# Performance work log

Measured on AMD Instinct MI355X. Metric: run time of the kernel, lower is better.

## Reference

```python
import jax, jax.numpy as jnp
import numpy as np

B, H, S, W, F = 16, 4, 8, 256, 16


def setup_inputs() -> dict:
    key = jax.random.key(0)
    kx, kk = jax.random.split(key)
    x = jax.random.normal(kx, (B, S, W, F), dtype=jnp.float32)
    kernel = jax.random.normal(kk, (H, S, S, W), dtype=jnp.float32)
    return {"x": x, "kernel": kernel}


def reference(x, kernel):
    # kernel: [H, S, S, W]; x: [B, S, W, F]
    Hh, Ss, _, Ww = kernel.shape
    r = jnp.arange(Ww)
    # stacked[h,x,y,j,i] = roll(kernel, shifts=j+1)[i] = kernel[(i-(j+1)) % W]
    idx = (r[None, :] - (r[:, None] + 1)) % Ww          # [W(row=j), W(col=i)]
    stacked = kernel[..., idx]                            # [H,S,S,W,W]
    # torch.tril over last two dims: keep col i <= row j
    tri = (r[None, :] <= r[:, None])                      # [W,W]
    stacked = jnp.where(tri, stacked, jnp.zeros((), dtype=stacked.dtype))
    # masked triangular time-mix contraction
    out = jnp.einsum('hxyji,bxif->bhxyjf', stacked, x)    # [B,H,S,S,W,F]
    base = jnp.arange(1, Ww + 1, dtype=out.dtype).reshape(1, 1, 1, 1, Ww, 1)
    out = out / base
    # transform_x: on diagonal series (x==y) roll time dim by 1, zero first step
    diag_mod = jnp.roll(out, 1, axis=4)
    not_first = (r != 0).reshape(1, 1, 1, 1, Ww, 1)
    diag_mod = diag_mod * not_first.astype(out.dtype)
    eye = jnp.eye(Ss, dtype=bool).reshape(1, 1, Ss, Ss, 1, 1)
    return jnp.where(eye, diag_mod, out)
```

## Files before the change

kernel.cpp:

```cpp
#include <hip/hip_runtime.h>
#include <hip/hip_bf16.h>

typedef short short8 __attribute__((ext_vector_type(8)));
typedef float f32x4 __attribute__((ext_vector_type(4)));

union FragAB { unsigned long long l[2]; int i[4]; short8 v; };

__global__ __launch_bounds__(256, 2)
void k_fused(const float* __restrict__ x,
             const float* __restrict__ kern,
             float* __restrict__ out)
{
    __shared__ __align__(16) ushort Xts[128 * 264];
    __shared__ __align__(8)  ushort wforL[2][4][336];

    const int blk = blockIdx.x;
    const int id = blk & 255;
    const int c  = id & 15;
    const int nt = (id >> 4) & 1;
    const int sx = id >> 5;
    const int mt = blk >> 8;

    const int t = threadIdx.x;

    #pragma unroll
    for (int e2 = 0; e2 < 2; ++e2) {
        const int hy = c * 2 + e2;
        const int h = hy >> 3, sy = hy & 7;
        const float* krow = kern + ((h * 8 + sx) * 8 + sy) * 256;
        #pragma unroll
        for (int s = 0; s < 4; ++s) {
            #pragma unroll
            for (int pass = 0; pass < 2; ++pass) {
                int q = t + pass * 256;
                if (q < 336) {
                    int src = q - s;
                    float v = (src >= 0 && src < 256) ? krow[src] : 0.0f;
                    __hip_bfloat16 hv = __float2bfloat16(v);
                    wforL[e2][s][q] = reinterpret_cast<ushort&>(hv);
                }
            }
        }
    }

    {
        const float4* xbase = reinterpret_cast<const float4*>(x);
        const int b0 = nt * 8;
        #pragma unroll
        for (int it = 0; it < 16; ++it) {
            int id4 = it * 256 + t;
            int fq = id4 & 3;
            int k2 = (id4 >> 2) & 127;
            int bl = id4 >> 9;
            const float4* rowp = xbase + ((size_t)((b0 + bl) * 8 + sx)) * 1024;
            float4 a = rowp[(2 * k2) * 4 + fq];
            float4 cq = rowp[(2 * k2 + 1) * 4 + fq];
            #pragma unroll
            for (int e = 0; e < 4; ++e) {
                float va = (&a.x)[e], vb = (&cq.x)[e];
                __hip_bfloat16 ha = __float2bfloat16(va);
                __hip_bfloat16 hb = __float2bfloat16(vb);
                uint u = (uint)reinterpret_cast<ushort&>(ha) |
                         ((uint)reinterpret_cast<ushort&>(hb) << 16);
                int row = bl * 16 + fq * 4 + e;
                *reinterpret_cast<uint*>(reinterpret_cast<char*>(Xts) + row * 528 + k2 * 4) = u;
            }
        }
    }
    __syncthreads();

    const int lane = t & 63, wid = t >> 6;
    const int wp = wid >> 1, wj = wid & 1;
    const int laneM = lane & 15, laneG = lane >> 4;
    const int wj0 = mt * 128 + wj * 64;
    const int kmax = wj0 + 64;

    const char* XtsB = reinterpret_cast<const char*>(Xts);
    const char* WB = reinterpret_cast<const char*>(wforL);
    const int abyte = (wp * 64 + laneM) * 528 + laneG * 16;

    #pragma unroll
    for (int e2 = 0; e2 < 2; ++e2) {
        const int hy = c * 2 + e2;
        const int h = hy >> 3, sy = hy & 7;
        const int diag = (sx == sy) ? 1 : 0;
        const int w00 = 255 + diag - wj0 - laneM + 8 * laneG;
        const int s = (laneM - diag + 1) & 3;
        const int bB = e2 * 2688 + s * 674 + 2 * w00;

        f32x4 acc[4][4];
        #pragma unroll
        for (int m = 0; m < 4; ++m)
            #pragma unroll
            for (int n = 0; n < 4; ++n)
                acc[m][n] = (f32x4){0.0f, 0.0f, 0.0f, 0.0f};

        for (int kc = 0; kc < kmax; kc += 32) {
            FragAB af[4];
            #pragma unroll
            for (int m = 0; m < 4; ++m) {
                const int4 raw = *reinterpret_cast<const int4*>(XtsB + abyte + m * 8448 + kc * 2);
                af[m].i[0] = raw.x; af[m].i[1] = raw.y;
                af[m].i[2] = raw.z; af[m].i[3] = raw.w;
            }
            FragAB bf[4];
            #pragma unroll
            for (int n = 0; n < 4; ++n) {
                const char* p = WB + bB + kc * 2 - 32 * n;
                bf[n].l[0] = *reinterpret_cast<const unsigned long long*>(p);
                bf[n].l[1] = *reinterpret_cast<const unsigned long long*>(p + 8);
            }
            #pragma unroll
            for (int m = 0; m < 4; ++m)
                #pragma unroll
                for (int n = 0; n < 4; ++n)
                    acc[m][n] = __builtin_amdgcn_mfma_f32_16x16x32_bf16(
                        af[m].v, bf[n].v, acc[m][n], 0, 0, 0);
        }

        #pragma unroll
        for (int n = 0; n < 4; ++n) {
            const int j = wj0 + 16 * n + laneM;
            const int denom = j + 1 - diag;
            const float rt = (denom > 0) ? (1.0f / (float)denom) : 0.0f;
            #pragma unroll
            for (int m = 0; m < 4; ++m) {
                const int b_ = nt * 8 + wp * 4 + m;
                float* dst = out + ((((size_t)(b_ * 4 + h) * 8 + sx) * 8 + sy) * 256 + j) * 16
                             + laneG * 4;
                float4 v;
                v.x = acc[m][n][0] * rt;
                v.y = acc[m][n][1] * rt;
                v.z = acc[m][n][2] * rt;
                v.w = acc[m][n][3] * rt;
                *reinterpret_cast<float4*>(dst) = v;
            }
        }
    }
}

extern "C" void kernel_launch(void* const* d_in, const int* in_sizes, int n_in,
                              void* d_out, int out_size, void* d_ws, size_t ws_size,
                              hipStream_t stream) {
    const float* x    = (const float*)d_in[0];
    const float* kern = (const float*)d_in[1];
    float* out = (float*)d_out;

    k_fused<<<512, 256, 0, stream>>>(x, kern, out);
}
```

Before: 22.14 us.

## Repartition work: one (h,sy) per block, 4 batches, full j range per wave

Each block now handles a single (h,sy) pair and four batches instead of two pairs and eight batches. Each of the four waves covers 64 j-columns over the full 256 range, so the grid doubles to 1024 blocks. This halves LDS use per block, allowing occupancy of 3 blocks per CU, and adds a shared-memory reciprocal table for the 1/(j+1) scaling. The trade-off is that the x tile is reloaded from global memory for each (h,sy) pair. Work across waves is also more imbalanced, because the triangular K range is now per-wave rather than paired across an mt split.

```diff
diff --git a/kernel.cpp b/kernel.cpp
--- a/kernel.cpp
+++ b/kernel.cpp
@@ -6,27 +6,24 @@
 
 union FragAB { unsigned long long l[2]; int i[4]; short8 v; };
 
-__global__ __launch_bounds__(256, 2)
+__global__ __launch_bounds__(256, 3)
 void k_fused(const float* __restrict__ x,
              const float* __restrict__ kern,
              float* __restrict__ out)
 {
-    __shared__ __align__(16) ushort Xts[128 * 264];
-    __shared__ __align__(8)  ushort wforL[2][4][336];
+    __shared__ __align__(16) ushort Xts[64 * 264];
+    __shared__ __align__(8)  ushort wforL[4][336];
+    __shared__ float rtab[256];
 
     const int blk = blockIdx.x;
-    const int id = blk & 255;
-    const int c  = id & 15;
-    const int nt = (id >> 4) & 1;
-    const int sx = id >> 5;
-    const int mt = blk >> 8;
-
+    const int hy = blk & 31;
+    const int sx = (blk >> 5) & 7;
+    const int nt = blk >> 8;
+    const int h = hy >> 3, sy = hy & 7;
+    const int diag = (sx == sy) ? 1 : 0;
     const int t = threadIdx.x;
 
-    #pragma unroll
-    for (int e2 = 0; e2 < 2; ++e2) {
-        const int hy = c * 2 + e2;
-        const int h = hy >> 3, sy = hy & 7;
+    {
         const float* krow = kern + ((h * 8 + sx) * 8 + sy) * 256;
         #pragma unroll
         for (int s = 0; s < 4; ++s) {
@@ -37,22 +34,24 @@
                     int src = q - s;
                     float v = (src >= 0 && src < 256) ? krow[src] : 0.0f;
                     __hip_bfloat16 hv = __float2bfloat16(v);
-                    wforL[e2][s][q] = reinterpret_cast<ushort&>(hv);
+                    wforL[s][q] = reinterpret_cast<ushort&>(hv);
                 }
             }
         }
     }
-
+    {
+        int denom = t + 1 - diag;
+        rtab[t] = (denom > 0) ? (1.0f / (float)denom) : 0.0f;
+    }
     {
         const float4* xbase = reinterpret_cast<const float4*>(x);
-        const int b0 = nt * 8;
         #pragma unroll
-        for (int it = 0; it < 16; ++it) {
-            int id4 = it * 256 + t;
-            int fq = id4 & 3;
-            int k2 = (id4 >> 2) & 127;
-            int bl = id4 >> 9;
-            const float4* rowp = xbase + ((size_t)((b0 + bl) * 8 + sx)) * 1024;
+        for (int it = 0; it < 8; ++it) {
+            int id = it * 256 + t;
+            int fq = id & 3;
+            int k2 = (id >> 2) & 127;
+            int bl = id >> 9;
+            const float4* rowp = xbase + ((size_t)((nt * 4 + bl) * 8 + sx)) * 1024;
             float4 a = rowp[(2 * k2) * 4 + fq];
             float4 cq = rowp[(2 * k2 + 1) * 4 + fq];
             #pragma unroll
@@ -70,71 +69,63 @@
     __syncthreads();
 
     const int lane = t & 63, wid = t >> 6;
-    const int wp = wid >> 1, wj = wid & 1;
     const int laneM = lane & 15, laneG = lane >> 4;
-    const int wj0 = mt * 128 + wj * 64;
+    const int wj0 = wid * 64;
     const int kmax = wj0 + 64;
 
     const char* XtsB = reinterpret_cast<const char*>(Xts);
     const char* WB = reinterpret_cast<const char*>(wforL);
-    const int abyte = (wp * 64 + laneM) * 528 + laneG * 16;
+    const int abyte = laneM * 528 + laneG * 16;
 
+    const int w00 = 255 + diag - wj0 - laneM + 8 * laneG;
+    const int s = (laneM - diag + 1) & 3;
+    const int bB = s * 674 + 2 * w00;
+
+    f32x4 acc[4][4];
     #pragma unroll
-    for (int e2 = 0; e2 < 2; ++e2) {
-        const int hy = c * 2 + e2;
-        const int h = hy >> 3, sy = hy & 7;
-        const int diag = (sx == sy) ? 1 : 0;
-        const int w00 = 255 + diag - wj0 - laneM + 8 * laneG;
-        const int s = (laneM - diag + 1) & 3;
-        const int bB = e2 * 2688 + s * 674 + 2 * w00;
+    for (int m = 0; m < 4; ++m)
+        #pragma unroll
+        for (int n = 0; n < 4; ++n)
+            acc[m][n] = (f32x4){0.0f, 0.0f, 0.0f, 0.0f};
 
-        f32x4 acc[4][4];
+    for (int kc = 0; kc < kmax; kc += 32) {
+        FragAB af[4];
+        #pragma unroll
+        for (int m = 0; m < 4; ++m) {
+            const int4 raw = *reinterpret_cast<const int4*>(XtsB + abyte + m * 8448 + kc * 2);
+            af[m].i[0] = raw.x; af[m].i[1] = raw.y;
+            af[m].i[2] = raw.z; af[m].i[3] = raw.w;
+        }
+        FragAB bf[4];
+        #pragma unroll
+        for (int n = 0; n < 4; ++n) {
+            const char* p = WB + bB + kc * 2 - 32 * n;
+            bf[n].l[0] = *reinterpret_cast<const unsigned long long*>(p);
+            bf[n].l[1] = *reinterpret_cast<const unsigned long long*>(p + 8);
+        }
         #pragma unroll
         for (int m = 0; m < 4; ++m)
             #pragma unroll
             for (int n = 0; n < 4; ++n)
-                acc[m][n] = (f32x4){0.0f, 0.0f, 0.0f, 0.0f};
+                acc[m][n] = __builtin_amdgcn_mfma_f32_16x16x32_bf16(
+                    af[m].v, bf[n].v, acc[m][n], 0, 0, 0);
+    }
 
-        for (int kc = 0; kc < kmax; kc += 32) {
-            FragAB af[4];
-            #pragma unroll
-            for (int m = 0; m < 4; ++m) {
-                const int4 raw = *reinterpret_cast<const int4*>(XtsB + abyte + m * 8448 + kc * 2);
-                af[m].i[0] = raw.x; af[m].i[1] = raw.y;
-                af[m].i[2] = raw.z; af[m].i[3] = raw.w;
-            }
-            FragAB bf[4];
-            #pragma unroll
-            for (int n = 0; n < 4; ++n) {
-                const char* p = WB + bB + kc * 2 - 32 * n;
-                bf[n].l[0] = *reinterpret_cast<const unsigned long long*>(p);
-                bf[n].l[1] = *reinterpret_cast<const unsigned long long*>(p + 8);
-            }
-            #pragma unroll
-            for (int m = 0; m < 4; ++m)
-                #pragma unroll
-                for (int n = 0; n < 4; ++n)
-                    acc[m][n] = __builtin_amdgcn_mfma_f32_16x16x32_bf16(
-                        af[m].v, bf[n].v, acc[m][n], 0, 0, 0);
-        }
-
+    #pragma unroll
+    for (int m = 0; m < 4; ++m) {
+        const int b_ = nt * 4 + m;
+        float* obase = out + (((size_t)(b_ * 4 + h) * 8 + sx) * 8 + sy) * 4096
+                       + laneG * 4;
         #pragma unroll
         for (int n = 0; n < 4; ++n) {
             const int j = wj0 + 16 * n + laneM;
-            const int denom = j + 1 - diag;
-            const float rt = (denom > 0) ? (1.0f / (float)denom) : 0.0f;
-            #pragma unroll
-            for (int m = 0; m < 4; ++m) {
-                const int b_ = nt * 8 + wp * 4 + m;
-                float* dst = out + ((((size_t)(b_ * 4 + h) * 8 + sx) * 8 + sy) * 256 + j) * 16
-                             + laneG * 4;
-                float4 v;
-                v.x = acc[m][n][0] * rt;
-                v.y = acc[m][n][1] * rt;
-                v.z = acc[m][n][2] * rt;
-                v.w = acc[m][n][3] * rt;
-                *reinterpret_cast<float4*>(dst) = v;
-            }
+            const float rt = rtab[j];
+            float4 v;
+            v.x = acc[m][n][0] * rt;
+            v.y = acc[m][n][1] * rt;
+            v.z = acc[m][n][2] * rt;
+            v.w = acc[m][n][3] * rt;
+            *reinterpret_cast<float4*>(obase + (size_t)j * 16) = v;
         }
     }
 }
@@ -146,5 +137,5 @@
     const float* kern = (const float*)d_in[1];
     float* out = (float*)d_out;
 
-    k_fused<<<512, 256, 0, stream>>>(x, kern, out);
+    k_fused<<<1024, 256, 0, stream>>>(x, kern, out);
 }
```

Result: faster. 20.92 us (-5.5%).
